# Kernel tuning notes

Measured on AMD Instinct MI355X. Metric: run time of the kernel, lower is better.

## Reference

```python
import jax, jax.numpy as jnp
import numpy as np
import math

D = 1024
H = 16
HD = D // H  # 64
SCALE = math.sqrt(HD)


def setup_inputs() -> dict:
    key = jax.random.key(0)
    ks = jax.random.split(key, 4)
    B, S = 2, 2048
    x = jax.random.normal(ks[0], (B, S, D), dtype=jnp.float32)
    attention_mask = jnp.zeros((B, S), dtype=jnp.float32)  # additive mask
    w_attn = jax.random.normal(ks[1], (D, 3 * D), dtype=jnp.float32) * (1.0 / math.sqrt(D))
    b_attn = jnp.zeros((3 * D,), dtype=jnp.float32)
    w_proj = jax.random.normal(ks[2], (D, D), dtype=jnp.float32) * (1.0 / math.sqrt(D))
    b_proj = jnp.zeros((D,), dtype=jnp.float32)
    return {"x": x, "attention_mask": attention_mask, "w_attn": w_attn,
            "b_attn": b_attn, "w_proj": w_proj, "b_proj": b_proj}


def reference(x, attention_mask, w_attn, b_attn, w_proj, b_proj):
    B, S, _ = x.shape
    qkv = x @ w_attn + b_attn                      # [B,S,3D]
    q, k, v = jnp.split(qkv, 3, axis=-1)           # each [B,S,D]
    # split heads -> [B,H,S,HD]
    sh = lambda t: t.reshape(B, S, H, HD).transpose(0, 2, 1, 3)
    q, k, v = sh(q), sh(k), sh(v)
    scores = jnp.einsum('bhqd,bhkd->bhqk', q, k) / SCALE   # [B,H,S,S]
    scores = scores + attention_mask[:, None, None, :]      # additive mask [B,1,1,S]
    attn = jax.nn.softmax(scores, axis=-1)                  # dropout disabled (eval)
    out = jnp.einsum('bhqk,bhkd->bhqd', attn, v)            # [B,H,S,HD]
    out = out.transpose(0, 2, 1, 3).reshape(B, S, D)        # merge heads
    out = out @ w_proj + b_proj                              # resid dropout disabled
    return out
```

## Files before the change

kernel.cpp:

```cpp
#include <hip/hip_runtime.h>
#include <math.h>

#define B_  2
#define S_  2048
#define D_  1024
#define H_  16
#define HD_ 64
#define BS_ (B_ * S_)

typedef float f32x4 __attribute__((ext_vector_type(4)));
typedef int   i32x4 __attribute__((ext_vector_type(4)));

__device__ __forceinline__ float bf2f(unsigned short u) {
    union { unsigned int i; float f; } c; c.i = ((unsigned int)u) << 16; return c.f;
}
__device__ __forceinline__ unsigned short f2bf(float f) {
    union { float f; unsigned int i; } c; c.f = f;
    unsigned int r = c.i + 0x7FFFu + ((c.i >> 16) & 1u);
    return (unsigned short)(r >> 16);
}
__device__ __forceinline__ unsigned int cvtpk_bf16(float lo, float hi) {
    unsigned int r;
    asm volatile("v_cvt_pk_bf16_f32 %0, %1, %2" : "=v"(r) : "v"(lo), "v"(hi));
    return r;
}
__device__ __forceinline__ void gl_lds16(const void* g, void* l) {
    __builtin_amdgcn_global_load_lds((const __attribute__((address_space(1))) void*)g,
                                     (__attribute__((address_space(3))) void*)l, 16, 0, 0);
}
__device__ __forceinline__ void mfma_bf16(f32x4& d, i32x4 a, i32x4 b) {
    asm volatile("v_mfma_f32_16x16x32_bf16 %0, %1, %2, %0" : "+v"(d) : "v"(a), "v"(b));
}

__global__ __launch_bounds__(256) void convert_f32_bf16(
    const float* __restrict__ in, unsigned short* __restrict__ out, int n)
{
    const int i = (blockIdx.x * 256 + threadIdx.x) * 8;
    if (i >= n) return;
    const float4 a = *reinterpret_cast<const float4*>(in + i);
    const float4 b = *reinterpret_cast<const float4*>(in + i + 4);
    ushort4 u0 = make_ushort4(f2bf(a.x), f2bf(a.y), f2bf(a.z), f2bf(a.w));
    ushort4 u1 = make_ushort4(f2bf(b.x), f2bf(b.y), f2bf(b.z), f2bf(b.w));
    *reinterpret_cast<ushort4*>(out + i)     = u0;
    *reinterpret_cast<ushort4*>(out + i + 4) = u1;
}

__global__ __launch_bounds__(256) void transpose_cvt(
    const float* __restrict__ W, unsigned short* __restrict__ Wt, int K, int N)
{
    __shared__ float t[32][33];
    const int n0 = blockIdx.x * 32, k0 = blockIdx.y * 32;
    const int tx = threadIdx.x & 31, ty = threadIdx.x >> 5;
#pragma unroll
    for (int r = 0; r < 32; r += 8)
        t[ty + r][tx] = W[(size_t)(k0 + ty + r) * N + n0 + tx];
    __syncthreads();
#pragma unroll
    for (int r = 0; r < 32; r += 8)
        Wt[(size_t)(n0 + ty + r) * K + k0 + tx] = f2bf(t[tx][ty + r]);
}

template <typename OutT, int BN>
__global__ __launch_bounds__(256) void gemm_bt_bf16(
    const unsigned short* __restrict__ A,
    const unsigned short* __restrict__ Bt,
    const float* __restrict__ bias,
    OutT* __restrict__ C, int M, int N, int K)
{
    constexpr int NW = BN / 2;
    constexpr int NI = NW / 16;
    __shared__ alignas(16) unsigned short As[2][4096];
    __shared__ alignas(16) unsigned short Bs[2][BN * 32];

    const int tid  = threadIdx.x;
    const int wave = tid >> 6;
    const int l    = tid & 63;
    const int g    = l >> 4;
    const int r    = l & 15;
    const int wr   = wave >> 1, wc = wave & 1;
    const int row0 = blockIdx.y * 128;
    const int col0 = blockIdx.x * BN;

    const size_t aoff0 = (size_t)(row0 +   0 + l) * K + wave * 8;
    const size_t aoff1 = (size_t)(row0 +  64 + l) * K + wave * 8;
    const size_t boff0 = (size_t)(col0 +   0 + l) * K + wave * 8;
    const size_t boff1 = (size_t)(col0 +  64 + l) * K + wave * 8;

    auto stage = [&](int kt, int buf) {
        gl_lds16(A + aoff0 + kt, &As[buf][wave * 1024]);
        gl_lds16(A + aoff1 + kt, &As[buf][wave * 1024 + 512]);
        if constexpr (BN == 128) {
            gl_lds16(Bt + boff0 + kt, &Bs[buf][wave * 1024]);
            gl_lds16(Bt + boff1 + kt, &Bs[buf][wave * 1024 + 512]);
        } else {
            gl_lds16(Bt + boff0 + kt, &Bs[buf][wave * 512]);
        }
    };

    f32x4 acc[4][NI];
#pragma unroll
    for (int mi = 0; mi < 4; ++mi)
#pragma unroll
        for (int ni = 0; ni < NI; ++ni) acc[mi][ni] = (f32x4)0.f;

    stage(0, 0);
    __syncthreads();

    for (int kt = 0; kt < K; kt += 32) {
        const int cur = (kt >> 5) & 1;
        if (kt + 32 < K) stage(kt + 32, cur ^ 1);

        const unsigned short* Ab = &As[cur][g * 1024];
        const unsigned short* Bb = &Bs[cur][g * (BN * 8)];
        i32x4 af[4], bf[NI];
#pragma unroll
        for (int mi = 0; mi < 4; ++mi)
            af[mi] = *reinterpret_cast<const i32x4*>(Ab + (wr * 64 + mi * 16 + r) * 8);
#pragma unroll
        for (int ni = 0; ni < NI; ++ni)
            bf[ni] = *reinterpret_cast<const i32x4*>(Bb + (wc * NW + ni * 16 + r) * 8);
#pragma unroll
        for (int mi = 0; mi < 4; ++mi)
#pragma unroll
            for (int ni = 0; ni < NI; ++ni)
                mfma_bf16(acc[mi][ni], af[mi], bf[ni]);

        __syncthreads();
    }

#pragma unroll
    for (int ni = 0; ni < NI; ++ni) {
        const int n = col0 + wc * NW + ni * 16 + r;
        const float bv = bias[n];
#pragma unroll
        for (int mi = 0; mi < 4; ++mi) {
#pragma unroll
            for (int e = 0; e < 4; ++e) {
                const int m = row0 + wr * 64 + mi * 16 + g * 4 + e;
                const float val = acc[mi][ni][e] + bv;
                if constexpr (sizeof(OutT) == 2)
                    C[(size_t)m * N + n] = (OutT)f2bf(val);
                else
                    C[(size_t)m * N + n] = (OutT)val;
            }
        }
    }
}

__global__ __launch_bounds__(512) void flash_attn_mfma(
    const unsigned short* __restrict__ qkv,
    const float* __restrict__ mask,
    unsigned short* __restrict__ out)
{
    __shared__ alignas(16) unsigned short Klds[2][4096];
    __shared__ alignas(16) unsigned short Vt[2][4096];

    const int tid  = threadIdx.x;
    const int wave = tid >> 6;
    const int l    = tid & 63;
    const int g    = l >> 4;
    const int r    = l & 15;
    const int b    = blockIdx.z;
    const int h    = blockIdx.y;
    const int q0   = blockIdx.x * 128;
    const int qw   = q0 + wave * 16;

    const size_t rs = 3 * (size_t)D_;
    const unsigned short* qb = qkv + (size_t)b * S_ * rs + (size_t)h * HD_;
    const unsigned short* kb = qb + D_;
    const unsigned short* vb = qb + 2 * D_;
    const float* mrow = mask + (size_t)b * S_;

    i32x4 qf[2];
#pragma unroll
    for (int ks = 0; ks < 2; ++ks)
        qf[ks] = *reinterpret_cast<const i32x4*>(
            qb + (size_t)(qw + r) * rs + ks * 32 + g * 8);

    const int kkey = (wave & 3) * 16 + (l >> 3);
    const int kuni = ((l & 7) ^ (l >> 3)) * 8;
    const int vkey = (wave & 3) * 16 + (l >> 2);
    const int vpart = l & 3;

    ushort4 vr[4];
    auto vload = [&](int kt) {
#pragma unroll
        for (int p = 0; p < 4; ++p)
            vr[p] = *reinterpret_cast<const ushort4*>(
                vb + (size_t)(kt + vkey) * rs + p * 16 + vpart * 4);
    };
    auto vwrite = [&](int buf) {
#pragma unroll
        for (int p = 0; p < 4; ++p) {
            const int d0 = p * 16 + vpart * 4;
            Vt[buf][(d0 + 0) * 64 + (vkey ^ (((d0 + 0) & 7) << 3))] = vr[p].x;
            Vt[buf][(d0 + 1) * 64 + (vkey ^ (((d0 + 1) & 7) << 3))] = vr[p].y;
            Vt[buf][(d0 + 2) * 64 + (vkey ^ (((d0 + 2) & 7) << 3))] = vr[p].z;
            Vt[buf][(d0 + 3) * 64 + (vkey ^ (((d0 + 3) & 7) << 3))] = vr[p].w;
        }
    };

    f32x4 acc[4];
    float m_i = -1e30f, l_i = 0.f;
#pragma unroll
    for (int mi = 0; mi < 4; ++mi) acc[mi] = (f32x4)0.f;

    if (wave < 4) {
        gl_lds16(kb + (size_t)(0 + kkey) * rs + kuni,     &Klds[0][(wave & 3) * 1024]);
        gl_lds16(kb + (size_t)(0 + kkey + 8) * rs + kuni, &Klds[0][(wave & 3) * 1024 + 512]);
    } else {
        vload(0);
        vwrite(0);
        vload(64);
    }
    __syncthreads();

    for (int kt = 0; kt < S_; kt += 64) {
        const int cur = (kt >> 6) & 1;
        if (wave < 4) {
            if (kt + 64 < S_) {
                gl_lds16(kb + (size_t)(kt + 64 + kkey) * rs + kuni,
                         &Klds[cur ^ 1][(wave & 3) * 1024]);
                gl_lds16(kb + (size_t)(kt + 64 + kkey + 8) * rs + kuni,
                         &Klds[cur ^ 1][(wave & 3) * 1024 + 512]);
            }
        } else {
            if (kt + 64 < S_) vwrite(cur ^ 1);
            if (kt + 128 < S_) vload(kt + 128);
        }

        const unsigned short* Kb = Klds[cur];
        const unsigned short* Vb = Vt[cur];

        f32x4 s[4];
#pragma unroll
        for (int mi = 0; mi < 4; ++mi) s[mi] = (f32x4)0.f;
#pragma unroll
        for (int ks = 0; ks < 2; ++ks)
#pragma unroll
            for (int mi = 0; mi < 4; ++mi) {
                const i32x4 kf = *reinterpret_cast<const i32x4*>(
                    Kb + (mi * 16 + r) * 64 + ((ks * 32 + g * 8) ^ ((r & 7) << 3)));
                mfma_bf16(s[mi], kf, qf[ks]);
            }

#pragma unroll
        for (int mi = 0; mi < 4; ++mi) {
            const float4 mk = *reinterpret_cast<const float4*>(
                mrow + kt + mi * 16 + g * 4);
            s[mi][0] = s[mi][0] * 0.125f + mk.x;
            s[mi][1] = s[mi][1] * 0.125f + mk.y;
            s[mi][2] = s[mi][2] * 0.125f + mk.z;
            s[mi][3] = s[mi][3] * 0.125f + mk.w;
        }

        float tmax = -1e30f;
#pragma unroll
        for (int mi = 0; mi < 4; ++mi)
#pragma unroll
            for (int e = 0; e < 4; ++e)
                tmax = fmaxf(tmax, s[mi][e]);
        tmax = fmaxf(tmax, __shfl_xor(tmax, 16));
        tmax = fmaxf(tmax, __shfl_xor(tmax, 32));
        const float mnew = fmaxf(m_i, tmax);
        const float corr = __expf(m_i - mnew);
        m_i = mnew;

        unsigned int pk[4][2];
        float ls = 0.f;
#pragma unroll
        for (int mi = 0; mi < 4; ++mi) {
            const float p0 = __expf(s[mi][0] - mnew);
            const float p1 = __expf(s[mi][1] - mnew);
            const float p2 = __expf(s[mi][2] - mnew);
            const float p3 = __expf(s[mi][3] - mnew);
            ls += (p0 + p1) + (p2 + p3);
            pk[mi][0] = cvtpk_bf16(p0, p1);
            pk[mi][1] = cvtpk_bf16(p2, p3);
        }
        l_i = l_i * corr + ls;
#pragma unroll
        for (int mi = 0; mi < 4; ++mi) acc[mi] *= corr;

#pragma unroll
        for (int ks = 0; ks < 2; ++ks) {
            i32x4 pf;
#pragma unroll
            for (int w = 0; w < 4; ++w) {
                const int src = (((g & 1) * 2 + (w >> 1)) << 4) + r;
                const unsigned int vA = __shfl(pk[2 * ks + 0][w & 1], src);
                const unsigned int vB = __shfl(pk[2 * ks + 1][w & 1], src);
                pf[w] = (int)((g >> 1) ? vB : vA);
            }
#pragma unroll
            for (int mi = 0; mi < 4; ++mi) {
                const i32x4 vf = *reinterpret_cast<const i32x4*>(
                    Vb + (mi * 16 + r) * 64 + ((ks * 32 + g * 8) ^ ((r & 7) << 3)));
                mfma_bf16(acc[mi], vf, pf);
            }
        }

        __syncthreads();
    }

    float lf = l_i;
    lf += __shfl_xor(lf, 16);
    lf += __shfl_xor(lf, 32);
    const float inv = 1.0f / lf;
    const size_t token = (size_t)b * S_ + qw + r;
#pragma unroll
    for (int mi = 0; mi < 4; ++mi) {
        const f32x4 v = acc[mi] * inv;
        uint2 w;
        w.x = cvtpk_bf16(v[0], v[1]);
        w.y = cvtpk_bf16(v[2], v[3]);
        *reinterpret_cast<uint2*>(
            out + token * D_ + h * HD_ + mi * 16 + g * 4) = w;
    }
}

extern "C" void kernel_launch(void* const* d_in, const int* in_sizes, int n_in,
                              void* d_out, int out_size, void* d_ws, size_t ws_size,
                              hipStream_t stream)
{
    const float* x      = (const float*)d_in[0];
    const float* amask  = (const float*)d_in[1];
    const float* w_attn = (const float*)d_in[2];
    const float* b_attn = (const float*)d_in[3];
    const float* w_proj = (const float*)d_in[4];
    const float* b_proj = (const float*)d_in[5];
    float* out = (float*)d_out;

    unsigned short* qkvb  = (unsigned short*)d_ws;
    unsigned short* attnb = qkvb  + (size_t)BS_ * 3 * D_;
    unsigned short* xb    = attnb + (size_t)BS_ * D_;
    unsigned short* wat   = xb    + (size_t)BS_ * D_;
    unsigned short* wpt   = wat   + (size_t)3 * D_ * D_;

    convert_f32_bf16<<<(BS_ * D_) / 2048, 256, 0, stream>>>(x, xb, BS_ * D_);
    transpose_cvt<<<dim3(3 * D_ / 32, D_ / 32), 256, 0, stream>>>(w_attn, wat, D_, 3 * D_);
    transpose_cvt<<<dim3(D_ / 32, D_ / 32), 256, 0, stream>>>(w_proj, wpt, D_, D_);

    gemm_bt_bf16<unsigned short, 128><<<dim3(3 * D_ / 128, BS_ / 128), 256, 0, stream>>>(
        xb, wat, b_attn, qkvb, BS_, 3 * D_, D_);

    flash_attn_mfma<<<dim3(S_ / 128, H_, B_), 512, 0, stream>>>(qkvb, amask, attnb);

    gemm_bt_bf16<float, 64><<<dim3(D_ / 64, BS_ / 128), 256, 0, stream>>>(
        attnb, wpt, b_proj, out, BS_, D_, D_);
}
```

Baseline: 172.5 us.

## Spread K/V tile loading across all attention waves and widen weight transpose

The flash-attention kernel used to split its eight waves into K loaders and V loaders, so half the waves did all the global-to-LDS K copies and the other half did all the V transposes. Now every wave loads half of a K slice and transposes half of the V columns, which evens out the per-wave prologue work and cuts V register staging. The weight transpose kernel moves to 64x64 tiles and writes four packed bf16 values per store to reduce store count. The max reduction is also rewritten as vector-wise maxes, a minor change.

```diff
diff --git a/kernel.cpp b/kernel.cpp
--- a/kernel.cpp
+++ b/kernel.cpp
@@ -30,6 +30,12 @@
 }
 __device__ __forceinline__ void mfma_bf16(f32x4& d, i32x4 a, i32x4 b) {
     asm volatile("v_mfma_f32_16x16x32_bf16 %0, %1, %2, %0" : "+v"(d) : "v"(a), "v"(b));
+}
+__device__ __forceinline__ f32x4 vmax4(f32x4 a, f32x4 b) {
+    f32x4 r;
+    r[0] = fmaxf(a[0], b[0]); r[1] = fmaxf(a[1], b[1]);
+    r[2] = fmaxf(a[2], b[2]); r[3] = fmaxf(a[3], b[3]);
+    return r;
 }
 
 __global__ __launch_bounds__(256) void convert_f32_bf16(
@@ -45,19 +51,25 @@
     *reinterpret_cast<ushort4*>(out + i + 4) = u1;
 }
 
-__global__ __launch_bounds__(256) void transpose_cvt(
+__global__ __launch_bounds__(256) void transpose_cvt64(
     const float* __restrict__ W, unsigned short* __restrict__ Wt, int K, int N)
 {
-    __shared__ float t[32][33];
-    const int n0 = blockIdx.x * 32, k0 = blockIdx.y * 32;
-    const int tx = threadIdx.x & 31, ty = threadIdx.x >> 5;
-#pragma unroll
-    for (int r = 0; r < 32; r += 8)
-        t[ty + r][tx] = W[(size_t)(k0 + ty + r) * N + n0 + tx];
+    __shared__ float t[64][65];
+    const int n0 = blockIdx.x * 64, k0 = blockIdx.y * 64;
+    const int tx = threadIdx.x & 63, ty = threadIdx.x >> 6;
+#pragma unroll
+    for (int kk = 0; kk < 64; kk += 4)
+        t[kk + ty][tx] = W[(size_t)(k0 + kk + ty) * N + n0 + tx];
     __syncthreads();
-#pragma unroll
-    for (int r = 0; r < 32; r += 8)
-        Wt[(size_t)(n0 + ty + r) * K + k0 + tx] = f2bf(t[tx][ty + r]);
+    const int nrow = threadIdx.x >> 2;
+    const int kq   = (threadIdx.x & 3) * 4;
+#pragma unroll
+    for (int p = 0; p < 4; ++p) {
+        const int k = p * 16 + kq;
+        ushort4 v = make_ushort4(f2bf(t[k + 0][nrow]), f2bf(t[k + 1][nrow]),
+                                 f2bf(t[k + 2][nrow]), f2bf(t[k + 3][nrow]));
+        *reinterpret_cast<ushort4*>(Wt + (size_t)(n0 + nrow) * K + k0 + k) = v;
+    }
 }
 
 template <typename OutT, int BN>
@@ -177,26 +189,28 @@
         qf[ks] = *reinterpret_cast<const i32x4*>(
             qb + (size_t)(qw + r) * rs + ks * 32 + g * 8);
 
-    const int kkey = (wave & 3) * 16 + (l >> 3);
+    const int kkey = (wave & 3) * 16 + (wave >> 2) * 8 + (l >> 3);
+    const int kdst = (wave & 3) * 1024 + (wave >> 2) * 512;
     const int kuni = ((l & 7) ^ (l >> 3)) * 8;
     const int vkey = (wave & 3) * 16 + (l >> 2);
     const int vpart = l & 3;
-
-    ushort4 vr[4];
+    const int vp0  = (wave >> 2) * 2;
+
+    ushort4 vr[2];
     auto vload = [&](int kt) {
 #pragma unroll
-        for (int p = 0; p < 4; ++p)
-            vr[p] = *reinterpret_cast<const ushort4*>(
-                vb + (size_t)(kt + vkey) * rs + p * 16 + vpart * 4);
+        for (int q = 0; q < 2; ++q)
+            vr[q] = *reinterpret_cast<const ushort4*>(
+                vb + (size_t)(kt + vkey) * rs + (vp0 + q) * 16 + vpart * 4);
     };
     auto vwrite = [&](int buf) {
 #pragma unroll
-        for (int p = 0; p < 4; ++p) {
-            const int d0 = p * 16 + vpart * 4;
-            Vt[buf][(d0 + 0) * 64 + (vkey ^ (((d0 + 0) & 7) << 3))] = vr[p].x;
-            Vt[buf][(d0 + 1) * 64 + (vkey ^ (((d0 + 1) & 7) << 3))] = vr[p].y;
-            Vt[buf][(d0 + 2) * 64 + (vkey ^ (((d0 + 2) & 7) << 3))] = vr[p].z;
-            Vt[buf][(d0 + 3) * 64 + (vkey ^ (((d0 + 3) & 7) << 3))] = vr[p].w;
+        for (int q = 0; q < 2; ++q) {
+            const int d0 = (vp0 + q) * 16 + vpart * 4;
+            Vt[buf][(d0 + 0) * 64 + (vkey ^ (((d0 + 0) & 7) << 3))] = vr[q].x;
+            Vt[buf][(d0 + 1) * 64 + (vkey ^ (((d0 + 1) & 7) << 3))] = vr[q].y;
+            Vt[buf][(d0 + 2) * 64 + (vkey ^ (((d0 + 2) & 7) << 3))] = vr[q].z;
+            Vt[buf][(d0 + 3) * 64 + (vkey ^ (((d0 + 3) & 7) << 3))] = vr[q].w;
         }
     };
 
@@ -205,29 +219,20 @@
 #pragma unroll
     for (int mi = 0; mi < 4; ++mi) acc[mi] = (f32x4)0.f;
 
-    if (wave < 4) {
-        gl_lds16(kb + (size_t)(0 + kkey) * rs + kuni,     &Klds[0][(wave & 3) * 1024]);
-        gl_lds16(kb + (size_t)(0 + kkey + 8) * rs + kuni, &Klds[0][(wave & 3) * 1024 + 512]);
-    } else {
-        vload(0);
-        vwrite(0);
-        vload(64);
-    }
+    gl_lds16(kb + (size_t)(0 + kkey) * rs + kuni, &Klds[0][kdst]);
+    vload(0);
+    vwrite(0);
+    vload(64);
     __syncthreads();
 
     for (int kt = 0; kt < S_; kt += 64) {
         const int cur = (kt >> 6) & 1;
-        if (wave < 4) {
-            if (kt + 64 < S_) {
-                gl_lds16(kb + (size_t)(kt + 64 + kkey) * rs + kuni,
-                         &Klds[cur ^ 1][(wave & 3) * 1024]);
-                gl_lds16(kb + (size_t)(kt + 64 + kkey + 8) * rs + kuni,
-                         &Klds[cur ^ 1][(wave & 3) * 1024 + 512]);
-            }
-        } else {
-            if (kt + 64 < S_) vwrite(cur ^ 1);
-            if (kt + 128 < S_) vload(kt + 128);
-        }
+        if (kt + 64 < S_) {
+            gl_lds16(kb + (size_t)(kt + 64 + kkey) * rs + kuni,
+                     &Klds[cur ^ 1][kdst]);
+            vwrite(cur ^ 1);
+        }
+        if (kt + 128 < S_) vload(kt + 128);
 
         const unsigned short* Kb = Klds[cur];
         const unsigned short* Vb = Vt[cur];
@@ -254,12 +259,8 @@
             s[mi][3] = s[mi][3] * 0.125f + mk.w;
         }
 
-        float tmax = -1e30f;
-#pragma unroll
-        for (int mi = 0; mi < 4; ++mi)
-#pragma unroll
-            for (int e = 0; e < 4; ++e)
-                tmax = fmaxf(tmax, s[mi][e]);
+        f32x4 m4 = vmax4(vmax4(s[0], s[1]), vmax4(s[2], s[3]));
+        float tmax = fmaxf(fmaxf(m4[0], m4[1]), fmaxf(m4[2], m4[3]));
         tmax = fmaxf(tmax, __shfl_xor(tmax, 16));
         tmax = fmaxf(tmax, __shfl_xor(tmax, 32));
         const float mnew = fmaxf(m_i, tmax);
@@ -338,8 +339,8 @@
     unsigned short* wpt   = wat   + (size_t)3 * D_ * D_;
 
     convert_f32_bf16<<<(BS_ * D_) / 2048, 256, 0, stream>>>(x, xb, BS_ * D_);
-    transpose_cvt<<<dim3(3 * D_ / 32, D_ / 32), 256, 0, stream>>>(w_attn, wat, D_, 3 * D_);
-    transpose_cvt<<<dim3(D_ / 32, D_ / 32), 256, 0, stream>>>(w_proj, wpt, D_, D_);
+    transpose_cvt64<<<dim3(3 * D_ / 64, D_ / 64), 256, 0, stream>>>(w_attn, wat, D_, 3 * D_);
+    transpose_cvt64<<<dim3(D_ / 64, D_ / 64), 256, 0, stream>>>(w_proj, wpt, D_, D_);
 
     gemm_bt_bf16<unsigned short, 128><<<dim3(3 * D_ / 128, BS_ / 128), 256, 0, stream>>>(
         xb, wat, b_attn, qkvb, BS_, 3 * D_, D_);
```

New measurement: 186.1 us. 7.9% more time.
